# Optimization experiments

Hardware: AMD Instinct MI355X
Metric: run time of the kernel (lower is better)

The kernel has to match this reference:

```python
import jax, jax.numpy as jnp
import numpy as np

# Module hyperparameters (from init_kwargs)
DT_W = 0.1
TAU_W = 10.0
ALPHA_W = DT_W / TAU_W                      # 0.01
SIGMA_W = float(np.sqrt(2.0 / ALPHA_W) * 0.01)  # sqrt(2/alpha) * sigma_w
WEIGHT_BOUND = 1.0
B, OUT, IN = 64, 1024, 1024


def setup_inputs() -> dict:
    key = jax.random.key(0)
    k_w, k_b, k_pre, k_post, k_kappa, k_noise = jax.random.split(key, 6)
    return {
        "w": jax.random.uniform(k_w, (B, OUT, IN), dtype=jnp.float32),
        "baseline": jax.random.uniform(k_b, (OUT, IN), dtype=jnp.float32),
        "R": jnp.ones((B, 1, 1), dtype=jnp.float32),
        "pre": jax.random.uniform(k_pre, (B, IN), dtype=jnp.float32),
        "post": jax.random.uniform(k_post, (B, OUT), dtype=jnp.float32),
        "kappa": jax.random.uniform(k_kappa, (OUT, IN), dtype=jnp.float32),
        "noise": jax.random.normal(k_noise, (B, OUT, IN), dtype=jnp.float32),
    }


def reference(w, baseline, R, pre, post, kappa, noise):
    # hebb[b,o,i] = post[b,o] * pre[b,i]  (rank-1 outer product per batch)
    hebb = jnp.einsum("bo,bi->boi", post, pre)
    eff_lr = jnp.abs(kappa)                      # plas_mask is None
    new_w = (baseline * ALPHA_W
             + w * (1.0 - ALPHA_W)
             + R * eff_lr * (hebb + SIGMA_W * noise))
    # clamp to [lb, ub] = [0, weight_bound]
    return jnp.clip(new_w, 0.0, WEIGHT_BOUND)
```

## Files before the change

### kernel.cpp

```cpp
#include <hip/hip_runtime.h>


constexpr int B_DIM  = 64;
constexpr int OUT_D  = 1024;
constexpr int IN_D   = 1024;
constexpr int IN4    = IN_D / 4;
constexpr float ALPHA  = 0.01f;
constexpr float ONE_MA = 1.0f - ALPHA;
constexpr float SIGMA  = 0.14142135623730951f;

__global__ __launch_bounds__(256)
void PlasticSynapse_69466801045994_kernel(
    const float4* __restrict__ w,
    const float4* __restrict__ baseline,
    const float*  __restrict__ R,
    const float4* __restrict__ pre,
    const float*  __restrict__ post,
    const float4* __restrict__ kappa,
    const float4* __restrict__ noise,
    float4*       __restrict__ out)
{
    const int idx = blockIdx.x * blockDim.x + threadIdx.x;

    const int i4 = idx & (IN4 - 1);
    const int bo = idx >> 8;
    const int o  = bo & (OUT_D - 1);
    const int b  = bo >> 10;

    const int oi = o * IN4 + i4;

    const float4 wv = w[idx];
    const float4 nv = noise[idx];
    const float4 bl = baseline[oi];
    const float4 kp = kappa[oi];
    const float4 pr = pre[b * IN4 + i4];
    const float  po = post[b * OUT_D + o];
    const float  r  = R[b];

    float4 res;
    {
        float lr = r * fabsf(kp.x);
        float v  = bl.x * ALPHA + wv.x * ONE_MA + lr * (po * pr.x + SIGMA * nv.x);
        res.x = fminf(fmaxf(v, 0.0f), 1.0f);
    }
    {
        float lr = r * fabsf(kp.y);
        float v  = bl.y * ALPHA + wv.y * ONE_MA + lr * (po * pr.y + SIGMA * nv.y);
        res.y = fminf(fmaxf(v, 0.0f), 1.0f);
    }
    {
        float lr = r * fabsf(kp.z);
        float v  = bl.z * ALPHA + wv.z * ONE_MA + lr * (po * pr.z + SIGMA * nv.z);
        res.z = fminf(fmaxf(v, 0.0f), 1.0f);
    }
    {
        float lr = r * fabsf(kp.w);
        float v  = bl.w * ALPHA + wv.w * ONE_MA + lr * (po * pr.w + SIGMA * nv.w);
        res.w = fminf(fmaxf(v, 0.0f), 1.0f);
    }

    out[idx] = res;
}

extern "C" void kernel_launch(void* const* d_in, const int* in_sizes, int n_in,
                              void* d_out, int out_size, void* d_ws, size_t ws_size,
                              hipStream_t stream) {
    const float4* w        = (const float4*)d_in[0];
    const float4* baseline = (const float4*)d_in[1];
    const float*  R        = (const float*) d_in[2];
    const float4* pre      = (const float4*)d_in[3];
    const float*  post     = (const float*) d_in[4];
    const float4* kappa    = (const float4*)d_in[5];
    const float4* noise    = (const float4*)d_in[6];
    float4*       out      = (float4*)d_out;

    const int total_vec = B_DIM * OUT_D * IN4;
    const int block = 256;
    const int grid  = total_vec / block;

    PlasticSynapse_69466801045994_kernel<<<grid, block, 0, stream>>>(
        w, baseline, R, pre, post, kappa, noise, out);
}
```

Measured before the change: 582.7 us.

## Use grid-stride loop over batch to reuse baseline/kappa and add nontemporal stores

```diff
diff --git a/kernel.cpp b/kernel.cpp
--- a/kernel.cpp
+++ b/kernel.cpp
@@ -5,11 +5,19 @@
 constexpr int OUT_D  = 1024;
 constexpr int IN_D   = 1024;
 constexpr int IN4    = IN_D / 4;
+constexpr int TOTAL4 = B_DIM * OUT_D * IN4;
+constexpr int BLOCK  = 256;
+constexpr int GRID   = 2048;
+constexpr int NTH    = BLOCK * GRID;
+constexpr int ITERS  = TOTAL4 / NTH;
+
 constexpr float ALPHA  = 0.01f;
 constexpr float ONE_MA = 1.0f - ALPHA;
 constexpr float SIGMA  = 0.14142135623730951f;
 
-__global__ __launch_bounds__(256)
+typedef float f32x4 __attribute__((ext_vector_type(4)));
+
+__global__ __launch_bounds__(BLOCK)
 void PlasticSynapse_69466801045994_kernel(
     const float4* __restrict__ w,
     const float4* __restrict__ baseline,
@@ -20,46 +28,50 @@
     const float4* __restrict__ noise,
     float4*       __restrict__ out)
 {
-    const int idx = blockIdx.x * blockDim.x + threadIdx.x;
+    const int tid = blockIdx.x * BLOCK + threadIdx.x;
 
-    const int i4 = idx & (IN4 - 1);
-    const int bo = idx >> 8;
-    const int o  = bo & (OUT_D - 1);
-    const int b  = bo >> 10;
+    const int i4  = tid & (IN4 - 1);
+    const int bo0 = tid >> 8;
+    const int o   = bo0 & (OUT_D - 1);
+    const int b0  = bo0 >> 10;
+    const int oi  = o * IN4 + i4;
 
-    const int oi = o * IN4 + i4;
-
-    const float4 wv = w[idx];
-    const float4 nv = noise[idx];
     const float4 bl = baseline[oi];
     const float4 kp = kappa[oi];
-    const float4 pr = pre[b * IN4 + i4];
-    const float  po = post[b * OUT_D + o];
-    const float  r  = R[b];
+    float4 blA, ak;
+    blA.x = bl.x * ALPHA;  blA.y = bl.y * ALPHA;
+    blA.z = bl.z * ALPHA;  blA.w = bl.w * ALPHA;
+    ak.x  = fabsf(kp.x);   ak.y  = fabsf(kp.y);
+    ak.z  = fabsf(kp.z);   ak.w  = fabsf(kp.w);
 
-    float4 res;
-    {
-        float lr = r * fabsf(kp.x);
-        float v  = bl.x * ALPHA + wv.x * ONE_MA + lr * (po * pr.x + SIGMA * nv.x);
-        res.x = fminf(fmaxf(v, 0.0f), 1.0f);
+#pragma unroll 4
+    for (int k = 0; k < ITERS; ++k) {
+        const int idx = tid + k * NTH;
+        const int b   = b0 + 2 * k;
+
+        const float4 wv = w[idx];
+        const float4 nv = noise[idx];
+        const float4 pr = pre[b * IN4 + i4];
+        const float  po = post[b * OUT_D + o];
+        const float  r  = R[b];
+
+        const float lrx = r * ak.x;
+        const float lry = r * ak.y;
+        const float lrz = r * ak.z;
+        const float lrw = r * ak.w;
+
+        float4 res;
+        res.x = fminf(fmaxf(fmaf(lrx, fmaf(SIGMA, nv.x, po * pr.x),
+                                 fmaf(wv.x, ONE_MA, blA.x)), 0.0f), 1.0f);
+        res.y = fminf(fmaxf(fmaf(lry, fmaf(SIGMA, nv.y, po * pr.y),
+                                 fmaf(wv.y, ONE_MA, blA.y)), 0.0f), 1.0f);
+        res.z = fminf(fmaxf(fmaf(lrz, fmaf(SIGMA, nv.z, po * pr.z),
+                                 fmaf(wv.z, ONE_MA, blA.z)), 0.0f), 1.0f);
+        res.w = fminf(fmaxf(fmaf(lrw, fmaf(SIGMA, nv.w, po * pr.w),
+                                 fmaf(wv.w, ONE_MA, blA.w)), 0.0f), 1.0f);
+
+        __builtin_nontemporal_store(*(const f32x4*)&res, (f32x4*)&out[idx]);
     }
-    {
-        float lr = r * fabsf(kp.y);
-        float v  = bl.y * ALPHA + wv.y * ONE_MA + lr * (po * pr.y + SIGMA * nv.y);
-        res.y = fminf(fmaxf(v, 0.0f), 1.0f);
-    }
-    {
-        float lr = r * fabsf(kp.z);
-        float v  = bl.z * ALPHA + wv.z * ONE_MA + lr * (po * pr.z + SIGMA * nv.z);
-        res.z = fminf(fmaxf(v, 0.0f), 1.0f);
-    }
-    {
-        float lr = r * fabsf(kp.w);
-        float v  = bl.w * ALPHA + wv.w * ONE_MA + lr * (po * pr.w + SIGMA * nv.w);
-        res.w = fminf(fmaxf(v, 0.0f), 1.0f);
-    }
-
-    out[idx] = res;
 }
 
 extern "C" void kernel_launch(void* const* d_in, const int* in_sizes, int n_in,
@@ -74,10 +86,6 @@
     const float4* noise    = (const float4*)d_in[6];
     float4*       out      = (float4*)d_out;
 
-    const int total_vec = B_DIM * OUT_D * IN4;
-    const int block = 256;
-    const int grid  = total_vec / block;
-
-    PlasticSynapse_69466801045994_kernel<<<grid, block, 0, stream>>>(
+    PlasticSynapse_69466801045994_kernel<<<GRID, BLOCK, 0, stream>>>(
         w, baseline, R, pre, post, kappa, noise, out);
 }
```

Result: no change. 586.4 us (+0.6%).
